# Kernel optimization log

Measured on AMD Instinct MI355X. Metric: run time of the kernel, lower is better.

## Reference

```python
import jax, jax.numpy as jnp
import numpy as np

NF = 128                 # num_filters
C_STATE = NF * 3 // 2    # ODE state channels (output of conv_up_embed_1) = 192
EPS = 1e-5               # InstanceNorm2d eps
N_STEPS = 4              # fixed-step RK4 steps over t in [0, 1]
DT = 1.0 / N_STEPS

nl = jax.nn.softplus     # get_nonlinearity('softplus')


def instance_norm(x):
    # InstanceNorm2d(affine=False): normalize over (H, W) per (N, C)
    m = x.mean(axis=(2, 3), keepdims=True)
    v = x.var(axis=(2, 3), keepdims=True)
    return (x - m) * jax.lax.rsqrt(v + EPS)


def conv2d(x, w, b):
    y = jax.lax.conv_general_dilated(
        x, w, window_strides=(1, 1), padding='SAME',
        dimension_numbers=('NCHW', 'OIHW', 'NCHW'))
    return y + b[None, :, None, None]


def setup_inputs() -> dict:
    key = jax.random.key(0)
    ks = jax.random.split(key, 10)
    B, H, W = 4, 64, 64
    s = 0.05
    return {
        'x':    jax.random.normal(ks[0], (B, NF, H, W), jnp.float32),
        'skip': jax.random.normal(ks[1], (B, NF, 2 * H, 2 * W), jnp.float32),
        # InitialVelocity: 3x3 conv nf -> nf
        'iv_w': jax.random.normal(ks[2], (NF, NF, 3, 3), jnp.float32) * s,
        'iv_b': jax.random.normal(ks[3], (NF,), jnp.float32) * s,
        # conv_up_embed_1: 1x1 conv 3nf -> 3nf//2
        'up_w': jax.random.normal(ks[4], (C_STATE, 3 * NF, 1, 1), jnp.float32) * s,
        'up_b': jax.random.normal(ks[5], (C_STATE,), jnp.float32) * s,
        # ConvSODEFunc convs (second-order: dv/dt = f(z, v))
        'f1_w': jax.random.normal(ks[6], (C_STATE // 2, C_STATE, 3, 3), jnp.float32) * s,
        'f1_b': jax.random.normal(ks[7], (C_STATE // 2,), jnp.float32) * s,
        'f2_w': jax.random.normal(ks[8], (C_STATE // 2, C_STATE // 2, 3, 3), jnp.float32) * s,
        'f2_b': jax.random.normal(ks[9], (C_STATE // 2,), jnp.float32) * s,
    }


def _ode_f(y, f1_w, f1_b, f2_w, f2_b):
    # second-order ODE: state y = [z, v]; dz/dt = v, dv/dt = f(y)
    c = y.shape[1] // 2
    v = y[:, c:]
    u = nl(conv2d(instance_norm(y), f1_w, f1_b))   # [B, C/2, H, W]
    dv = nl(conv2d(instance_norm(u), f2_w, f2_b))  # [B, C/2, H, W]
    return jnp.concatenate([v, dv], axis=1)


def reference(x, skip, iv_w, iv_b, up_w, up_b, f1_w, f1_b, f2_w, f2_b):
    # InitialVelocity (counter == 0): concat learned velocity -> 2*nf channels
    v0 = nl(conv2d(instance_norm(x), iv_w, iv_b))
    y = jnp.concatenate([x, v0], axis=1)                       # [B, 2nf, H, W]
    B, C, H, W = y.shape
    # bilinear upsample x2, align_corners=False (half-pixel centers)
    y = jax.image.resize(y, (B, C, 2 * H, 2 * W), method='bilinear')
    y = jnp.concatenate([y, skip], axis=1)                     # [B, 3nf, 2H, 2W]
    y = nl(conv2d(y, up_w, up_b))                              # [B, 3nf//2, 2H, 2W]
    # ODEBlock: integrate t: 0 -> 1, fixed-step RK4 via lax.scan
    f = lambda s: _ode_f(s, f1_w, f1_b, f2_w, f2_b)

    def step(s, _):
        k1 = f(s)
        k2 = f(s + 0.5 * DT * k1)
        k3 = f(s + 0.5 * DT * k2)
        k4 = f(s + DT * k3)
        s = s + (DT / 6.0) * (k1 + 2.0 * k2 + 2.0 * k3 + k4)
        return s, None

    y, _ = jax.lax.scan(step, y, None, length=N_STEPS)
    return y
```

## Files before the change

kernel.cpp:

```cpp
#include <hip/hip_runtime.h>
#include <math.h>

#define BB 4
#define NF 128
#define CS 192
#define CH 96
#define H1 64
#define W1 64
#define H2 128
#define W2 128
#define P1 (H1*W1)
#define P2 (H2*W2)
#define EPSV 1e-5f
#define DTV 0.25f
#define NSLICE 32
#define SLOTSZ (1536 * NSLICE)

typedef __attribute__((ext_vector_type(8))) short short8;
typedef __attribute__((ext_vector_type(4))) float f32x4;

__device__ __forceinline__ float softplus_f(float x) {
    return fmaxf(x, 0.0f) + __logf(1.0f + __expf(-fabsf(x)));
}
__device__ __forceinline__ unsigned f2bf(float f) {
    unsigned u = __float_as_uint(f);
    return (u + 0x7FFFu + ((u >> 16) & 1u)) >> 16;
}
__device__ __forceinline__ float bf2f(short s) {
    return __uint_as_float(((unsigned)(unsigned short)s) << 16);
}
__device__ __forceinline__ int packbf(float a, float b) {
    return (int)(f2bf(a) | (f2bf(b) << 16));
}

__global__ __launch_bounds__(256) void zero_kernel(float* __restrict__ p, int n) {
    int i = blockIdx.x * 256 + threadIdx.x;
    if (i < n) p[i] = 0.f;
}

__global__ __launch_bounds__(256) void meanvar_raw_kernel(const float* __restrict__ x,
                                                          float* __restrict__ mv, int HW) {
    int bc = blockIdx.x;
    const float* p = x + (size_t)bc * HW;
    float s = 0.f, s2 = 0.f;
    for (int i = threadIdx.x; i < HW; i += 256) {
        float v = p[i];
        s += v; s2 += v * v;
    }
    __shared__ float sh[512];
    sh[threadIdx.x] = s; sh[256 + threadIdx.x] = s2;
    __syncthreads();
    for (int o = 128; o > 0; o >>= 1) {
        if (threadIdx.x < o) {
            sh[threadIdx.x] += sh[threadIdx.x + o];
            sh[256 + threadIdx.x] += sh[256 + threadIdx.x + o];
        }
        __syncthreads();
    }
    if (threadIdx.x == 0) {
        mv[2 * bc]     = sh[0];
        mv[2 * bc + 1] = sh[256];
    }
}

__global__ __launch_bounds__(256) void repack_w_kernel(const float* __restrict__ w,
                                                       short* __restrict__ wq,
                                                       int Cout, int Cin) {
    int idx = blockIdx.x * 256 + threadIdx.x;
    int total = Cout * Cin * 9;
    if (idx >= total) return;
    int tap = idx % 9;
    int t = idx / 9;
    int ci = t % Cin, co = t / Cin;
    int COGl = Cout >> 4;
    int cog = co >> 4, lx = co & 15;
    int it = ci >> 5, q = (ci >> 3) & 3, e = ci & 7;
    size_t o = (((size_t)(it * 9 + tap) * COGl + cog) * 64 + q * 16 + lx) * 8 + e;
    wq[o] = (short)f2bf(w[idx]);
}

__global__ __launch_bounds__(256) void repack_w1_kernel(const float* __restrict__ w,
                                                        short* __restrict__ wq,
                                                        int Cout, int Cin) {
    int idx = blockIdx.x * 256 + threadIdx.x;
    if (idx >= Cout * Cin) return;
    int ci = idx % Cin, co = idx / Cin;
    int COGl = Cout >> 4;
    int cog = co >> 4, lx = co & 15;
    int it = ci >> 5, q = (ci >> 3) & 3, e = ci & 7;
    size_t o = (((size_t)it * COGl + cog) * 64 + q * 16 + lx) * 8 + e;
    wq[o] = (short)f2bf(w[idx]);
}

__global__ __launch_bounds__(256) void xcvt_kernel(const float* __restrict__ x,
                                                   short* __restrict__ xbf) {
    __shared__ int buf[64 * 68];
    const int tid = threadIdx.x;
    const int px = tid & 63, jj = tid >> 6;
    const int px0 = blockIdx.x * 64;
    const int b = blockIdx.y;
#pragma unroll
    for (int ji = 0; ji < 16; ji++) {
        int j = jj + 4 * ji;
        int c = 2 * j;
        float a = x[((size_t)(b * NF + c)) * P1 + px0 + px];
        float d = x[((size_t)(b * NF + c + 1)) * P1 + px0 + px];
        buf[px * 68 + j] = packbf(a, d);
    }
    __syncthreads();
#pragma unroll
    for (int k = 0; k < 4; k++) {
        int idx = tid + 256 * k;
        int p2 = idx >> 4, w4 = idx & 15;
        int4 v = *(const int4*)&buf[p2 * 68 + w4 * 4];
        *(int4*)(xbf + ((size_t)b * P1 + px0 + p2) * NF + w4 * 8) = v;
    }
}

template<int CIN, int NCG, bool OUTBF, bool SUMS>
__global__ __launch_bounds__(256) void conv3x3_mfma(
    const short* __restrict__ in, const float* __restrict__ mvsums,
    const short* __restrict__ wq, const float* __restrict__ bias,
    float* __restrict__ outf, short* __restrict__ outbf, float* __restrict__ osum,
    int CoutT, int H, int W, int outC, int outCoff, int coblk)
{
    constexpr int ROWS = CIN + 8;
    constexpr int STGI = 180 * ROWS / 2;
    constexpr int SMEMI = (OUTBF && 128 * 52 > STGI) ? 128 * 52 : STGI;
    constexpr int NCGH = NCG / 2;
    __shared__ int smem[SMEMI];
    short* xt = (short*)smem;
    __shared__ float mvm[CIN], mvr[CIN];
    __shared__ float shs[2 * CH];
    const int tid = threadIdx.x;
    const int w4 = tid >> 6, lane = tid & 63;
    const int wy = w4 & 1, wc = w4 >> 1;
    const int lx = lane & 15, q = lane >> 4;
    const int x0 = blockIdx.x * 16, y0 = blockIdx.y * 8;
    const int b = blockIdx.z / coblk;
    const int co_base = (blockIdx.z % coblk) * (NCG * 16);
    const int slice = (blockIdx.x + (blockIdx.y << 3)) & (NSLICE - 1);
    const int HWp = H * W;
    const short* inb = in + (size_t)b * HWp * CIN;

    const float invHW = 1.0f / (float)HWp;
    for (int c = tid; c < CIN; c += 256) {
        float s = 0.f, s2 = 0.f;
#pragma unroll
        for (int sl = 0; sl < NSLICE; sl++) {
            s  += mvsums[(size_t)sl * 1536 + (b * CIN + c) * 2];
            s2 += mvsums[(size_t)sl * 1536 + (b * CIN + c) * 2 + 1];
        }
        float m  = s * invHW;
        float var = fmaxf(s2 * invHW - m * m, 0.f);
        mvm[c] = m;
        mvr[c] = rsqrtf(var + EPSV);
    }
    if (SUMS) for (int c = tid; c < 2 * CH; c += 256) shs[c] = 0.f;
    __syncthreads();

    constexpr int PARTS = CIN / 8;
    constexpr int TOT = 180 * PARTS;
    constexpr int NJ = (TOT + 255) / 256;
#pragma unroll
    for (int k = 0; k < NJ; k++) {
        int j = tid + 256 * k;
        if (j < TOT) {
            int px = j / PARTS, part = j - px * PARTS;
            int yy = px / 18, xx = px - yy * 18;
            int gy = y0 + yy - 1, gx = x0 + xx - 1;
            int4 wv = make_int4(0, 0, 0, 0);
            if (gy >= 0 && gy < H && gx >= 0 && gx < W) {
                int cb = part * 8;
                short8 v = *(const short8*)(inb + (size_t)(gy * W + gx) * CIN + cb);
                float4 m0 = *(const float4*)&mvm[cb];
                float4 m1 = *(const float4*)&mvm[cb + 4];
                float4 r0 = *(const float4*)&mvr[cb];
                float4 r1 = *(const float4*)&mvr[cb + 4];
                wv.x = packbf((bf2f(v[0]) - m0.x) * r0.x, (bf2f(v[1]) - m0.y) * r0.y);
                wv.y = packbf((bf2f(v[2]) - m0.z) * r0.z, (bf2f(v[3]) - m0.w) * r0.w);
                wv.z = packbf((bf2f(v[4]) - m1.x) * r1.x, (bf2f(v[5]) - m1.y) * r1.y);
                wv.w = packbf((bf2f(v[6]) - m1.z) * r1.z, (bf2f(v[7]) - m1.w) * r1.w);
            }
            *(int4*)(&xt[px * ROWS + part * 8]) = wv;
        }
    }
    __syncthreads();

    f32x4 acc[4][NCGH];
#pragma unroll
    for (int rr = 0; rr < 4; rr++)
#pragma unroll
        for (int cg = 0; cg < NCGH; cg++) acc[rr][cg] = (f32x4)(0.f);

    constexpr int NIT = CIN / 32;
    constexpr int NC = 9 * NIT;
    const int COGl = CoutT >> 4;
    const short* wbase = wq + ((size_t)((co_base >> 4) + wc * NCGH) * 64 + lane) * 8;
    const size_t wstep = (size_t)COGl * 512;

    auto ldw = [&](int c, short8* dst) {
#pragma unroll
        for (int cg = 0; cg < NCGH; cg++)
            dst[cg] = *(const short8*)(wbase + (size_t)c * wstep + (size_t)cg * 512);
    };
    auto body = [&](int c, const short8* a) {
        const int it = c / 9, tap = c - 9 * (c / 9);
        const int dy = tap / 3, dx = tap - 3 * (tap / 3);
        short8 bfr[4];
#pragma unroll
        for (int rr = 0; rr < 4; rr++)
            bfr[rr] = *(const short8*)(
                &xt[((wy * 4 + rr + dy) * 18 + lx + dx) * ROWS + it * 32 + q * 8]);
#pragma unroll
        for (int rr = 0; rr < 4; rr++)
#pragma unroll
            for (int cg = 0; cg < NCGH; cg++)
                acc[rr][cg] = __builtin_amdgcn_mfma_f32_16x16x32_bf16(
                    a[cg], bfr[rr], acc[rr][cg], 0, 0, 0);
    };

    short8 aA[NCGH], aB[NCGH], aC[NCGH];
    ldw(0, aA);
    ldw(1, aB);
#pragma unroll
    for (int c = 0; c < NC; c += 3) {
        if (c + 2 < NC) ldw(c + 2, aC);
        body(c, aA);
        if (c + 3 < NC) ldw(c + 3, aA);
        if (c + 1 < NC) body(c + 1, aB);
        if (c + 4 < NC) ldw(c + 4, aB);
        if (c + 2 < NC) body(c + 2, aC);
    }

    if (OUTBF) __syncthreads();

    float s1l[NCGH][4], s2l[NCGH][4];
    if (SUMS) {
#pragma unroll
        for (int cg = 0; cg < NCGH; cg++)
#pragma unroll
            for (int r = 0; r < 4; r++) { s1l[cg][r] = 0.f; s2l[cg][r] = 0.f; }
    }
#pragma unroll
    for (int rr = 0; rr < 4; rr++) {
        int y = y0 + wy * 4 + rr;
#pragma unroll
        for (int cg = 0; cg < NCGH; cg++) {
            float v[4];
#pragma unroll
            for (int r = 0; r < 4; r++) {
                int co = wc * (NCGH * 16) + cg * 16 + q * 4 + r;
                v[r] = softplus_f(acc[rr][cg][r] + bias[co_base + co]);
                if (SUMS) { s1l[cg][r] += v[r]; s2l[cg][r] += v[r] * v[r]; }
            }
            if (OUTBF) {
                int pl = (wy * 4 + rr) * 16 + lx;
                smem[pl * 52 + wc * (NCGH * 8) + cg * 8 + q * 2]     = packbf(v[0], v[1]);
                smem[pl * 52 + wc * (NCGH * 8) + cg * 8 + q * 2 + 1] = packbf(v[2], v[3]);
            } else {
                float* ob = outf + ((size_t)b * outC + outCoff + co_base) * HWp
                            + y * W + x0 + lx;
#pragma unroll
                for (int r = 0; r < 4; r++)
                    ob[(size_t)(wc * (NCGH * 16) + cg * 16 + q * 4 + r) * HWp] = v[r];
            }
        }
    }
    if (OUTBF) {
        __syncthreads();
#pragma unroll
        for (int k = 0; k < 6; k++) {
            int idx = tid + 256 * k;
            int pl2 = idx / 12, w4i = idx % 12;
            int4 v = *(const int4*)&smem[pl2 * 52 + w4i * 4];
            int pix = (y0 + (pl2 >> 4)) * W + x0 + (pl2 & 15);
            *(int4*)(outbf + ((size_t)b * HWp + pix) * 96 + w4i * 8) = v;
        }
    }
    if (SUMS) {
#pragma unroll
        for (int cg = 0; cg < NCGH; cg++)
#pragma unroll
            for (int r = 0; r < 4; r++) {
                float a1 = s1l[cg][r], a2 = s2l[cg][r];
#pragma unroll
                for (int mask = 1; mask < 16; mask <<= 1) {
                    a1 += __shfl_xor(a1, mask);
                    a2 += __shfl_xor(a2, mask);
                }
                if (lx == 0) {
                    int co = wc * (NCGH * 16) + cg * 16 + q * 4 + r;
                    atomicAdd(&shs[2 * co], a1);
                    atomicAdd(&shs[2 * co + 1], a2);
                }
            }
        __syncthreads();
        for (int c = tid; c < 2 * NCG * 16; c += 256)
            atomicAdd(&osum[(size_t)slice * 1536 + (size_t)b * 2 * NCG * 16 + c], shs[c]);
    }
}

__global__ __launch_bounds__(256, 8) void upsample_kernel(
    const float* __restrict__ x, const float* __restrict__ v0,
    const float* __restrict__ skip, short* __restrict__ ycat)
{
    __shared__ int buf[32 * 98];
    const int tid = threadIdx.x;
    const int px = tid & 31, jj = tid >> 5;
    const int px0 = blockIdx.x * 32;
    const int b = blockIdx.y;
    const int pxg = px0 + px;
    const int ox = pxg & 127, oy = pxg >> 7;
    int my = oy >> 1, mx = ox >> 1;
    int iy0 = (oy & 1) ? my : my - 1;
    float wy0 = (oy & 1) ? 0.75f : 0.25f;
    int ix0 = (ox & 1) ? mx : mx - 1;
    float wx0 = (ox & 1) ? 0.75f : 0.25f;
    int iy1 = min(iy0 + 1, H1 - 1); iy0 = max(iy0, 0);
    int ix1 = min(ix0 + 1, W1 - 1); ix0 = max(ix0, 0);
    float wy1 = 1.f - wy0, wx1 = 1.f - wx0;
    float w00 = wy0 * wx0, w01 = wy0 * wx1, w10 = wy1 * wx0, w11 = wy1 * wx1;
    int o00 = iy0 * W1 + ix0, o01 = iy0 * W1 + ix1;
    int o10 = iy1 * W1 + ix0, o11 = iy1 * W1 + ix1;

#pragma unroll
    for (int half = 0; half < 2; half++) {
        if (half == 1) __syncthreads();
#pragma unroll 4
        for (int ji = 0; ji < 12; ji++) {
            int j = jj + 8 * ji + half * 96;
            int c = 2 * j;
            float a, d;
            if (c < 256) {
                const float* s0 = (c < 128) ? x + ((size_t)(b * NF + c)) * P1
                                            : v0 + ((size_t)(b * NF + c - 128)) * P1;
                const float* s1 = s0 + P1;
                a = w00 * s0[o00] + w01 * s0[o01] + w10 * s0[o10] + w11 * s0[o11];
                d = w00 * s1[o00] + w01 * s1[o01] + w10 * s1[o10] + w11 * s1[o11];
            } else {
                const float* sk = skip + ((size_t)(b * NF + c - 256)) * P2 + pxg;
                a = sk[0]; d = sk[P2];
            }
            buf[px * 98 + (j - half * 96)] = packbf(a, d);
        }
        __syncthreads();
#pragma unroll
        for (int k = 0; k < 3; k++) {
            int idx = tid + 256 * k;
            int p2 = idx / 24, w4 = idx % 24;
            int4 v = *(const int4*)&buf[p2 * 98 + w4 * 4];
            *(int4*)(ycat + ((size_t)b * P2 + px0 + p2) * 384 + half * 192 + w4 * 8) = v;
        }
    }
}

__global__ __launch_bounds__(256, 4) void conv1x1_mfma(
    const short* __restrict__ ycat, const short* __restrict__ wq,
    const float* __restrict__ bias, float* __restrict__ out,
    short* __restrict__ sbf, float* __restrict__ osum)
{
    __shared__ int smem[64 * 100];
    short* xs = (short*)smem;
    const int tid = threadIdx.x;
    const int wave = tid >> 6, lane = tid & 63;
    const int lx = lane & 15, q = lane >> 4;
    const int p0 = blockIdx.x * 64;
    const int b = blockIdx.y;
    const int slice = blockIdx.x & (NSLICE - 1);

    f32x4 acc[3][4];
#pragma unroll
    for (int cg = 0; cg < 3; cg++)
#pragma unroll
        for (int pg = 0; pg < 4; pg++) acc[cg][pg] = (f32x4)(0.f);

    const short* wbase = wq + ((size_t)(wave * 3) * 64 + lane) * 8;
    auto ldw = [&](int it, short8* dst) {
#pragma unroll
        for (int cg = 0; cg < 3; cg++)
            dst[cg] = *(const short8*)(wbase + (size_t)(it * 12 + cg) * 512);
    };
    auto mbody = [&](int itl, const short8* a) {
        short8 bfr[4];
#pragma unroll
        for (int pg = 0; pg < 4; pg++)
            bfr[pg] = *(const short8*)(&xs[(pg * 16 + lx) * 200 + itl * 32 + q * 8]);
#pragma unroll
        for (int pg = 0; pg < 4; pg++)
#pragma unroll
            for (int cg = 0; cg < 3; cg++)
                acc[cg][pg] = __builtin_amdgcn_mfma_f32_16x16x32_bf16(
                    a[cg], bfr[pg], acc[cg][pg], 0, 0, 0);
    };

    const short* yb = ycat + ((size_t)b * P2 + p0) * 384;
#pragma unroll
    for (int half = 0; half < 2; half++) {
        if (half == 1) __syncthreads();
#pragma unroll
        for (int k = 0; k < 6; k++) {
            int j = tid + 256 * k;
            int spx = j / 24, spart = j - spx * 24;
            short8 v = *(const short8*)(yb + (size_t)spx * 384 + half * 192 + spart * 8);
            *(short8*)(&xs[spx * 200 + spart * 8]) = v;
        }
        __syncthreads();

        short8 aA[3], aB[3], aC[3];
        ldw(half * 6 + 0, aA);
        ldw(half * 6 + 1, aB);
#pragma unroll
        for (int c = 0; c < 6; c += 3) {
            ldw(half * 6 + c + 2, aC);
            mbody(c, aA);
            if (c + 3 < 6) ldw(half * 6 + c + 3, aA);
            mbody(c + 1, aB);
            if (c + 4 < 6) ldw(half * 6 + c + 4, aB);
            mbody(c + 2, aC);
        }
    }
    __syncthreads();

    float s1a[3][4], s2a[3][4];
#pragma unroll
    for (int cg = 0; cg < 3; cg++)
#pragma unroll
        for (int r = 0; r < 4; r++) { s1a[cg][r] = 0.f; s2a[cg][r] = 0.f; }
#pragma unroll
    for (int cg = 0; cg < 3; cg++) {
        int co0 = wave * 48 + cg * 16 + q * 4;
#pragma unroll
        for (int pg = 0; pg < 4; pg++) {
            int pl = pg * 16 + lx;
            float v[4];
#pragma unroll
            for (int r = 0; r < 4; r++) {
                v[r] = softplus_f(acc[cg][pg][r] + bias[co0 + r]);
                out[((size_t)(b * CS + co0 + r)) * P2 + p0 + pl] = v[r];
                s1a[cg][r] += v[r]; s2a[cg][r] += v[r] * v[r];
            }
            smem[pl * 100 + (co0 >> 1)]     = packbf(v[0], v[1]);
            smem[pl * 100 + (co0 >> 1) + 1] = packbf(v[2], v[3]);
        }
    }
    __syncthreads();
#pragma unroll
    for (int k = 0; k < 6; k++) {
        int idx = tid + 256 * k;
        int p2 = idx / 24, w4 = idx % 24;
        int4 v = *(const int4*)&smem[p2 * 100 + w4 * 4];
        *(int4*)(sbf + ((size_t)b * P2 + p0 + p2) * 192 + w4 * 8) = v;
    }
#pragma unroll
    for (int cg = 0; cg < 3; cg++)
#pragma unroll
        for (int r = 0; r < 4; r++) {
            float a1 = s1a[cg][r], a2 = s2a[cg][r];
#pragma unroll
            for (int mask = 1; mask < 16; mask <<= 1) {
                a1 += __shfl_xor(a1, mask);
                a2 += __shfl_xor(a2, mask);
            }
            if (lx == 0) {
                int co = wave * 48 + cg * 16 + q * 4 + r;
                atomicAdd(&osum[(size_t)slice * 1536 + ((size_t)b * CS + co) * 2], a1);
                atomicAdd(&osum[(size_t)slice * 1536 + ((size_t)b * CS + co) * 2 + 1], a2);
            }
        }
}

__global__ __launch_bounds__(256) void combine_kernel(
    const float* __restrict__ S, const float* __restrict__ Gx,
    const float* __restrict__ Gp, short* __restrict__ T, float* __restrict__ osum,
    float ca1, float ca2, float cb)
{
    __shared__ int buf[64 * 100];
    const int tid = threadIdx.x;
    const int px = tid & 63, jj = tid >> 6;
    const int px0 = blockIdx.x * 64;
    const int b = blockIdx.y;
    const int pxg = px0 + px;
    const int slice = blockIdx.x & (NSLICE - 1);
#pragma unroll 3
    for (int ji = 0; ji < 12; ji++) {
        int j = jj + 4 * ji;
        int c = 2 * j;
        size_t ia = ((size_t)(b * CS + c)) * P2 + pxg;
        size_t ib = ia + (size_t)CH * P2;
        size_t ig = ((size_t)(b * CH + c)) * P2 + pxg;
        float sa0 = S[ia], sa1 = S[ia + P2];
        float sb0 = S[ib], sb1 = S[ib + P2];
        float gx0 = Gx[ig], gx1 = Gx[ig + P2];
        float gp0 = Gp[ig], gp1 = Gp[ig + P2];
        buf[px * 100 + j]      = packbf(sa0 + ca1 * sb0 + ca2 * gx0,
                                        sa1 + ca1 * sb1 + ca2 * gx1);
        buf[px * 100 + 48 + j] = packbf(sb0 + cb * gp0, sb1 + cb * gp1);
    }
    __syncthreads();
#pragma unroll
    for (int k = 0; k < 6; k++) {
        int idx = tid + 256 * k;
        int p2 = idx / 24, w4 = idx % 24;
        int4 v = *(const int4*)&buf[p2 * 100 + w4 * 4];
        *(int4*)(T + ((size_t)b * P2 + px0 + p2) * 192 + w4 * 8) = v;
    }
    if (tid < 192) {
        int jj2 = tid >> 1, s = tid & 1;
        float s1lo = 0.f, s2lo = 0.f, s1hi = 0.f, s2hi = 0.f;
#pragma unroll 8
        for (int p = s; p < 64; p += 2) {
            int v = buf[p * 100 + jj2];
            float lo = bf2f((short)v), hi = bf2f((short)(v >> 16));
            s1lo += lo; s2lo += lo * lo; s1hi += hi; s2hi += hi * hi;
        }
        s1lo += __shfl_xor(s1lo, 1); s2lo += __shfl_xor(s2lo, 1);
        s1hi += __shfl_xor(s1hi, 1); s2hi += __shfl_xor(s2hi, 1);
        if (s == 0) {
            int c = 2 * jj2;
            float* dst = &osum[(size_t)slice * 1536 + ((size_t)b * CS + c) * 2];
            atomicAdd(dst, s1lo);
            atomicAdd(dst + 1, s2lo);
            atomicAdd(dst + 2, s1hi);
            atomicAdd(dst + 3, s2hi);
        }
    }
}

template<bool SBF>
__global__ __launch_bounds__(256) void final_kernel(
    float* __restrict__ S, const float* __restrict__ G1, const float* __restrict__ G2,
    const float* __restrict__ G3, const float* __restrict__ G4,
    short* __restrict__ sbf, float* __restrict__ osum)
{
    __shared__ int buf[SBF ? 64 * 100 : 4];
    const int tid = threadIdx.x;
    const int px = tid & 63, jj = tid >> 6;
    const int px0 = blockIdx.x * 64;
    const int b = blockIdx.y;
    const int pxg = px0 + px;
    const int slice = blockIdx.x & (NSLICE - 1);
    const float cA = DTV * DTV / 6.0f, cB = DTV / 6.0f;
#pragma unroll 3
    for (int ji = 0; ji < 12; ji++) {
        int j = jj + 4 * ji;
        int c = 2 * j;
        size_t ia = ((size_t)(b * CS + c)) * P2 + pxg;
        size_t ib = ia + (size_t)CH * P2;
        size_t ig = ((size_t)(b * CH + c)) * P2 + pxg;
        float sa0 = S[ia], sa1 = S[ia + P2];
        float sb0 = S[ib], sb1 = S[ib + P2];
        float g10 = G1[ig], g11 = G1[ig + P2];
        float g20 = G2[ig], g21 = G2[ig + P2];
        float g30 = G3[ig], g31 = G3[ig + P2];
        float g40 = G4[ig], g41 = G4[ig + P2];
        float na0 = sa0 + DTV * sb0 + cA * (g10 + g20 + g30);
        float na1 = sa1 + DTV * sb1 + cA * (g11 + g21 + g31);
        float nb0 = sb0 + cB * (g10 + 2.f * g20 + 2.f * g30 + g40);
        float nb1 = sb1 + cB * (g11 + 2.f * g21 + 2.f * g31 + g41);
        S[ia] = na0; S[ia + P2] = na1;
        S[ib] = nb0; S[ib + P2] = nb1;
        if (SBF) {
            buf[px * 100 + j]      = packbf(na0, na1);
            buf[px * 100 + 48 + j] = packbf(nb0, nb1);
        }
    }
    if (SBF) {
        __syncthreads();
#pragma unroll
        for (int k = 0; k < 6; k++) {
            int idx = tid + 256 * k;
            int p2 = idx / 24, w4 = idx % 24;
            int4 v = *(const int4*)&buf[p2 * 100 + w4 * 4];
            *(int4*)(sbf + ((size_t)b * P2 + px0 + p2) * 192 + w4 * 8) = v;
        }
        if (tid < 192) {
            int jj2 = tid >> 1, s = tid & 1;
            float s1lo = 0.f, s2lo = 0.f, s1hi = 0.f, s2hi = 0.f;
#pragma unroll 8
            for (int p = s; p < 64; p += 2) {
                int v = buf[p * 100 + jj2];
                float lo = bf2f((short)v), hi = bf2f((short)(v >> 16));
                s1lo += lo; s2lo += lo * lo; s1hi += hi; s2hi += hi * hi;
            }
            s1lo += __shfl_xor(s1lo, 1); s2lo += __shfl_xor(s2lo, 1);
            s1hi += __shfl_xor(s1hi, 1); s2hi += __shfl_xor(s2hi, 1);
            if (s == 0) {
                int c = 2 * jj2;
                float* dst = &osum[(size_t)slice * 1536 + ((size_t)b * CS + c) * 2];
                atomicAdd(dst, s1lo);
                atomicAdd(dst + 1, s2lo);
                atomicAdd(dst + 2, s1hi);
                atomicAdd(dst + 3, s2hi);
            }
        }
    }
}

extern "C" void kernel_launch(void* const* d_in, const int* in_sizes, int n_in,
                              void* d_out, int out_size, void* d_ws, size_t ws_size,
                              hipStream_t stream) {
    (void)in_sizes; (void)n_in; (void)out_size; (void)ws_size;
    const float* x    = (const float*)d_in[0];
    const float* skip = (const float*)d_in[1];
    const float* iv_w = (const float*)d_in[2];
    const float* iv_b = (const float*)d_in[3];
    const float* up_w = (const float*)d_in[4];
    const float* up_b = (const float*)d_in[5];
    const float* f1_w = (const float*)d_in[6];
    const float* f1_b = (const float*)d_in[7];
    const float* f2_w = (const float*)d_in[8];
    const float* f2_b = (const float*)d_in[9];

    float* S = (float*)d_out;
    float* ws = (float*)d_ws;
    const size_t NGf = (size_t)BB * CH * P2;
    float* G1 = ws;
    float* G2 = G1 + NGf;
    float* G3 = G2 + NGf;
    float* G4 = G3 + NGf;
    short* T   = (short*)(G4 + NGf);
    short* U   = T + (size_t)BB * P2 * CS;
    short* SBF = U + (size_t)BB * P2 * CH;
    float* MVS = (float*)(SBF + (size_t)BB * P2 * CS);
    short* IVQ = (short*)(MVS + (size_t)34 * SLOTSZ);
    short* F1Q = IVQ + (size_t)9 * NF * NF;
    short* F2Q = F1Q + (size_t)9 * CH * CS;
    short* UPQ = F2Q + (size_t)9 * CH * CH;
    short* YCAT = (short*)G1;
    float* V0   = G3;
    short* XBF  = (short*)G4;

    auto slot = [&](int i) { return MVS + (size_t)i * SLOTSZ; };

    zero_kernel<<<(34 * SLOTSZ + 255) / 256, 256, 0, stream>>>(MVS, 34 * SLOTSZ);
    repack_w_kernel<<<(NF * NF * 9 + 255) / 256, 256, 0, stream>>>(iv_w, IVQ, NF, NF);
    repack_w_kernel<<<(CH * CS * 9 + 255) / 256, 256, 0, stream>>>(f1_w, F1Q, CH, CS);
    repack_w_kernel<<<(CH * CH * 9 + 255) / 256, 256, 0, stream>>>(f2_w, F2Q, CH, CH);
    repack_w1_kernel<<<(CS * 384 + 255) / 256, 256, 0, stream>>>(up_w, UPQ, CS, 384);

    meanvar_raw_kernel<<<BB * NF, 256, 0, stream>>>(x, slot(0), P1);
    xcvt_kernel<<<dim3(P1 / 64, BB), 256, 0, stream>>>(x, XBF);
    conv3x3_mfma<128, 4, false, false><<<dim3(W1 / 16, H1 / 8, BB * 2), 256, 0, stream>>>(
        XBF, slot(0), IVQ, iv_b, V0, nullptr, nullptr, NF, H1, W1, NF, 0, 2);
    upsample_kernel<<<dim3(P2 / 32, BB), 256, 0, stream>>>(x, V0, skip, YCAT);
    conv1x1_mfma<<<dim3(P2 / 64, BB), 256, 0, stream>>>(YCAT, UPQ, up_b, S, SBF, slot(1));

    const float h = DTV;
    float* G[4] = {G1, G2, G3, G4};
    int sc = 2;
    float* yslot = slot(1);
    const dim3 egrd(P2 / 64, BB);

    for (int step = 0; step < 4; step++) {
        for (int sub = 0; sub < 4; sub++) {
            const short* Ybf = (sub == 0) ? SBF : T;
            float* uslot = slot(sc++);
            conv3x3_mfma<192, 6, true, true><<<dim3(W2 / 16, H2 / 8, BB), 256, 0, stream>>>(
                Ybf, yslot, F1Q, f1_b, nullptr, U, uslot, CH, H2, W2, CH, 0, 1);
            conv3x3_mfma<96, 6, false, false><<<dim3(W2 / 16, H2 / 8, BB), 256, 0, stream>>>(
                U, uslot, F2Q, f2_b, G[sub], nullptr, nullptr, CH, H2, W2, CH, 0, 1);
            if (sub < 3) {
                float ca1, ca2, cb;
                const float *Gx, *Gp;
                if (sub == 0)      { ca1 = h/2; ca2 = 0.f;     Gx = G1; Gp = G1; cb = h/2; }
                else if (sub == 1) { ca1 = h/2; ca2 = h*h/4;   Gx = G1; Gp = G2; cb = h/2; }
                else               { ca1 = h;   ca2 = h*h/2;   Gx = G2; Gp = G3; cb = h;   }
                float* tslot = slot(sc++);
                combine_kernel<<<egrd, 256, 0, stream>>>(S, Gx, Gp, T, tslot, ca1, ca2, cb);
                yslot = tslot;
            }
        }
        if (step < 3) {
            float* sslot = slot(sc++);
            final_kernel<true><<<egrd, 256, 0, stream>>>(S, G1, G2, G3, G4, SBF, sslot);
            yslot = sslot;
        } else {
            final_kernel<false><<<egrd, 256, 0, stream>>>(S, G1, G2, G3, G4, SBF, nullptr);
        }
    }
}
```

Baseline: 1.515 ms.

## Split conv3x3 input channels into LDS phases and widen upsample blocks

Adds a KS template parameter so the 192-channel f1 conv stages its input tile in two channel halves. This shrinks the LDS tile and lets more blocks fit per CU, with launch bounds now asking for 4 blocks per SM. Each half is loaded, normalized and consumed by MFMA before the next, at the cost of an extra barrier and a pipeline restart per half. The upsample kernel also moves to 64 pixels per block and drops its occupancy hint.

Result: slower. 1.624 ms (+7.2%).

```diff
diff --git a/kernel.cpp b/kernel.cpp
--- a/kernel.cpp
+++ b/kernel.cpp
@@ -117,14 +117,15 @@
     }
 }
 
-template<int CIN, int NCG, bool OUTBF, bool SUMS>
-__global__ __launch_bounds__(256) void conv3x3_mfma(
+template<int CIN, int KS, int NCG, bool OUTBF, bool SUMS>
+__global__ __launch_bounds__(256, 4) void conv3x3_mfma(
     const short* __restrict__ in, const float* __restrict__ mvsums,
     const short* __restrict__ wq, const float* __restrict__ bias,
     float* __restrict__ outf, short* __restrict__ outbf, float* __restrict__ osum,
     int CoutT, int H, int W, int outC, int outCoff, int coblk)
 {
-    constexpr int ROWS = CIN + 8;
+    constexpr int CINH = CIN / KS;
+    constexpr int ROWS = CINH + 8;
     constexpr int STGI = 180 * ROWS / 2;
     constexpr int SMEMI = (OUTBF && 128 * 52 > STGI) ? 128 * 52 : STGI;
     constexpr int NCGH = NCG / 2;
@@ -159,50 +160,25 @@
     if (SUMS) for (int c = tid; c < 2 * CH; c += 256) shs[c] = 0.f;
     __syncthreads();
 
-    constexpr int PARTS = CIN / 8;
+    constexpr int PARTS = CINH / 8;
     constexpr int TOT = 180 * PARTS;
     constexpr int NJ = (TOT + 255) / 256;
-#pragma unroll
-    for (int k = 0; k < NJ; k++) {
-        int j = tid + 256 * k;
-        if (j < TOT) {
-            int px = j / PARTS, part = j - px * PARTS;
-            int yy = px / 18, xx = px - yy * 18;
-            int gy = y0 + yy - 1, gx = x0 + xx - 1;
-            int4 wv = make_int4(0, 0, 0, 0);
-            if (gy >= 0 && gy < H && gx >= 0 && gx < W) {
-                int cb = part * 8;
-                short8 v = *(const short8*)(inb + (size_t)(gy * W + gx) * CIN + cb);
-                float4 m0 = *(const float4*)&mvm[cb];
-                float4 m1 = *(const float4*)&mvm[cb + 4];
-                float4 r0 = *(const float4*)&mvr[cb];
-                float4 r1 = *(const float4*)&mvr[cb + 4];
-                wv.x = packbf((bf2f(v[0]) - m0.x) * r0.x, (bf2f(v[1]) - m0.y) * r0.y);
-                wv.y = packbf((bf2f(v[2]) - m0.z) * r0.z, (bf2f(v[3]) - m0.w) * r0.w);
-                wv.z = packbf((bf2f(v[4]) - m1.x) * r1.x, (bf2f(v[5]) - m1.y) * r1.y);
-                wv.w = packbf((bf2f(v[6]) - m1.z) * r1.z, (bf2f(v[7]) - m1.w) * r1.w);
-            }
-            *(int4*)(&xt[px * ROWS + part * 8]) = wv;
-        }
-    }
-    __syncthreads();
-
-    f32x4 acc[4][NCGH];
-#pragma unroll
-    for (int rr = 0; rr < 4; rr++)
-#pragma unroll
-        for (int cg = 0; cg < NCGH; cg++) acc[rr][cg] = (f32x4)(0.f);
-
-    constexpr int NIT = CIN / 32;
-    constexpr int NC = 9 * NIT;
+    constexpr int NITH = CINH / 32;
+    constexpr int NCH = 9 * NITH;
     const int COGl = CoutT >> 4;
     const short* wbase = wq + ((size_t)((co_base >> 4) + wc * NCGH) * 64 + lane) * 8;
     const size_t wstep = (size_t)COGl * 512;
 
-    auto ldw = [&](int c, short8* dst) {
+    f32x4 acc[4][NCGH];
+#pragma unroll
+    for (int rr = 0; rr < 4; rr++)
+#pragma unroll
+        for (int cg = 0; cg < NCGH; cg++) acc[rr][cg] = (f32x4)(0.f);
+
+    auto ldw = [&](int gc, short8* dst) {
 #pragma unroll
         for (int cg = 0; cg < NCGH; cg++)
-            dst[cg] = *(const short8*)(wbase + (size_t)c * wstep + (size_t)cg * 512);
+            dst[cg] = *(const short8*)(wbase + (size_t)gc * wstep + (size_t)cg * 512);
     };
     auto body = [&](int c, const short8* a) {
         const int it = c / 9, tap = c - 9 * (c / 9);
@@ -220,17 +196,47 @@
                     a[cg], bfr[rr], acc[rr][cg], 0, 0, 0);
     };
 
-    short8 aA[NCGH], aB[NCGH], aC[NCGH];
-    ldw(0, aA);
-    ldw(1, aB);
-#pragma unroll
-    for (int c = 0; c < NC; c += 3) {
-        if (c + 2 < NC) ldw(c + 2, aC);
-        body(c, aA);
-        if (c + 3 < NC) ldw(c + 3, aA);
-        if (c + 1 < NC) body(c + 1, aB);
-        if (c + 4 < NC) ldw(c + 4, aB);
-        if (c + 2 < NC) body(c + 2, aC);
+#pragma unroll
+    for (int p = 0; p < KS; p++) {
+        if (p > 0) __syncthreads();
+#pragma unroll
+        for (int k = 0; k < NJ; k++) {
+            int j = tid + 256 * k;
+            if (j < TOT) {
+                int px = j / PARTS, part = j - px * PARTS;
+                int yy = px / 18, xx = px - yy * 18;
+                int gy = y0 + yy - 1, gx = x0 + xx - 1;
+                int4 wv = make_int4(0, 0, 0, 0);
+                if (gy >= 0 && gy < H && gx >= 0 && gx < W) {
+                    int cb = p * CINH + part * 8;
+                    short8 v = *(const short8*)(inb + (size_t)(gy * W + gx) * CIN + cb);
+                    float4 m0 = *(const float4*)&mvm[cb];
+                    float4 m1 = *(const float4*)&mvm[cb + 4];
+                    float4 r0 = *(const float4*)&mvr[cb];
+                    float4 r1 = *(const float4*)&mvr[cb + 4];
+                    wv.x = packbf((bf2f(v[0]) - m0.x) * r0.x, (bf2f(v[1]) - m0.y) * r0.y);
+                    wv.y = packbf((bf2f(v[2]) - m0.z) * r0.z, (bf2f(v[3]) - m0.w) * r0.w);
+                    wv.z = packbf((bf2f(v[4]) - m1.x) * r1.x, (bf2f(v[5]) - m1.y) * r1.y);
+                    wv.w = packbf((bf2f(v[6]) - m1.z) * r1.z, (bf2f(v[7]) - m1.w) * r1.w);
+                }
+                *(int4*)(&xt[px * ROWS + part * 8]) = wv;
+            }
+        }
+        __syncthreads();
+
+        const int gc0 = p * NCH;
+        short8 aA[NCGH], aB[NCGH], aC[NCGH];
+        ldw(gc0 + 0, aA);
+        ldw(gc0 + 1, aB);
+#pragma unroll
+        for (int c = 0; c < NCH; c += 3) {
+            if (c + 2 < NCH) ldw(gc0 + c + 2, aC);
+            body(c, aA);
+            if (c + 3 < NCH) ldw(gc0 + c + 3, aA);
+            if (c + 1 < NCH) body(c + 1, aB);
+            if (c + 4 < NCH) ldw(gc0 + c + 4, aB);
+            if (c + 2 < NCH) body(c + 2, aC);
+        }
     }
 
     if (OUTBF) __syncthreads();
@@ -301,14 +307,14 @@
     }
 }
 
-__global__ __launch_bounds__(256, 8) void upsample_kernel(
+__global__ __launch_bounds__(256) void upsample_kernel(
     const float* __restrict__ x, const float* __restrict__ v0,
     const float* __restrict__ skip, short* __restrict__ ycat)
 {
-    __shared__ int buf[32 * 98];
+    __shared__ int buf[64 * 98];
     const int tid = threadIdx.x;
-    const int px = tid & 31, jj = tid >> 5;
-    const int px0 = blockIdx.x * 32;
+    const int px = tid & 63, jj = tid >> 6;
+    const int px0 = blockIdx.x * 64;
     const int b = blockIdx.y;
     const int pxg = px0 + px;
     const int ox = pxg & 127, oy = pxg >> 7;
@@ -328,8 +334,8 @@
     for (int half = 0; half < 2; half++) {
         if (half == 1) __syncthreads();
 #pragma unroll 4
-        for (int ji = 0; ji < 12; ji++) {
-            int j = jj + 8 * ji + half * 96;
+        for (int ji = 0; ji < 24; ji++) {
+            int j = jj + 4 * ji + half * 96;
             int c = 2 * j;
             float a, d;
             if (c < 256) {
@@ -346,7 +352,7 @@
         }
         __syncthreads();
 #pragma unroll
-        for (int k = 0; k < 3; k++) {
+        for (int k = 0; k < 6; k++) {
             int idx = tid + 256 * k;
             int p2 = idx / 24, w4 = idx % 24;
             int4 v = *(const int4*)&buf[p2 * 98 + w4 * 4];
@@ -641,9 +647,9 @@
 
     meanvar_raw_kernel<<<BB * NF, 256, 0, stream>>>(x, slot(0), P1);
     xcvt_kernel<<<dim3(P1 / 64, BB), 256, 0, stream>>>(x, XBF);
-    conv3x3_mfma<128, 4, false, false><<<dim3(W1 / 16, H1 / 8, BB * 2), 256, 0, stream>>>(
+    conv3x3_mfma<128, 1, 4, false, false><<<dim3(W1 / 16, H1 / 8, BB * 2), 256, 0, stream>>>(
         XBF, slot(0), IVQ, iv_b, V0, nullptr, nullptr, NF, H1, W1, NF, 0, 2);
-    upsample_kernel<<<dim3(P2 / 32, BB), 256, 0, stream>>>(x, V0, skip, YCAT);
+    upsample_kernel<<<dim3(P2 / 64, BB), 256, 0, stream>>>(x, V0, skip, YCAT);
     conv1x1_mfma<<<dim3(P2 / 64, BB), 256, 0, stream>>>(YCAT, UPQ, up_b, S, SBF, slot(1));
 
     const float h = DTV;
@@ -656,9 +662,9 @@
         for (int sub = 0; sub < 4; sub++) {
             const short* Ybf = (sub == 0) ? SBF : T;
             float* uslot = slot(sc++);
-            conv3x3_mfma<192, 6, true, true><<<dim3(W2 / 16, H2 / 8, BB), 256, 0, stream>>>(
+            conv3x3_mfma<192, 2, 6, true, true><<<dim3(W2 / 16, H2 / 8, BB), 256, 0, stream>>>(
                 Ybf, yslot, F1Q, f1_b, nullptr, U, uslot, CH, H2, W2, CH, 0, 1);
-            conv3x3_mfma<96, 6, false, false><<<dim3(W2 / 16, H2 / 8, BB), 256, 0, stream>>>(
+            conv3x3_mfma<96, 1, 6, false, false><<<dim3(W2 / 16, H2 / 8, BB), 256, 0, stream>>>(
                 U, uslot, F2Q, f2_b, G[sub], nullptr, nullptr, CH, H2, W2, CH, 0, 1);
             if (sub < 3) {
                 float ca1, ca2, cb;
```
